# Kernel optimization log

Hardware: AMD Instinct MI355X
Metric: run time of the kernel (lower is better)

Reference implementation:

```python
import jax, jax.numpy as jnp
import numpy as np


def setup_inputs() -> dict:
    key = jax.random.key(0)
    ks = jax.random.split(key, 5)
    b, f, h, w, c = 2, 16, 64, 64, 256
    heads, D = 8, 32
    hD = heads * D
    x = jax.random.normal(ks[0], (b, f, h, w, c), dtype=jnp.float32)
    s = 1.0 / np.sqrt(c)
    Wq = jax.random.normal(ks[1], (c, hD), dtype=jnp.float32) * s
    Wk = jax.random.normal(ks[2], (c, hD), dtype=jnp.float32) * s
    Wv = jax.random.normal(ks[3], (c, hD), dtype=jnp.float32) * s
    Wo = jax.random.normal(ks[4], (hD, c), dtype=jnp.float32) * s
    return {"x": x, "Wq": Wq, "Wk": Wk, "Wv": Wv, "Wo": Wo, "heads": heads}


def reference(x, Wq, Wk, Wv, Wo, heads):
    b, f, h, w, c = x.shape
    hD = Wq.shape[1]
    D = hD // heads
    n = h * w
    # fuse batch & frames; 1x1 conv == channel matmul
    xf = x.reshape(b * f, n, c)  # [(bf), n, c]

    def proj(W):
        # [(bf), n, hD] -> [(bf), heads, D, n]
        p = jnp.einsum('bnc,cd->bnd', xf, W)
        return p.reshape(b * f, n, heads, D).transpose(0, 2, 3, 1)

    q = jax.nn.softmax(proj(Wq), axis=-2)  # softmax over D (note: scale is dead code in source)
    k = jax.nn.softmax(proj(Wk), axis=-1)  # softmax over spatial n
    v = proj(Wv)
    context = jnp.einsum('bhdn,bhen->bhde', k, v)      # [(bf), heads, D, D]
    out = jnp.einsum('bhde,bhdn->bhen', context, q)    # [(bf), heads, D, n]
    out = out.transpose(0, 3, 1, 2).reshape(b * f, n, hD)
    out = jnp.einsum('bnd,dc->bnc', out, Wo)
    return out.reshape(b, f, h, w, c)
```

## Files before the change

kernel.cpp:

```cpp
#include <hip/hip_runtime.h>
#include <hip/hip_bf16.h>


typedef __attribute__((ext_vector_type(8))) short bf16x8;
typedef __attribute__((ext_vector_type(4))) float f32x4;

__device__ __forceinline__ unsigned short f2bf(float x) {
  __hip_bfloat16 h = __float2bfloat16(x);
  union { __hip_bfloat16 b; unsigned short u; } c; c.b = h; return c.u;
}

__global__ __launch_bounds__(256) void k0_prep(const float* __restrict__ Wq,
                                               const float* __restrict__ Wk,
                                               const float* __restrict__ Wv,
                                               unsigned short* __restrict__ WqT,
                                               unsigned short* __restrict__ WkvT) {
  int r = blockIdx.x, c = threadIdx.x;
  if (r < 256)      WqT [(r      )*256 + c] = f2bf(Wq[c*256 + r]);
  else if (r < 512) WkvT[(r - 256)*256 + c] = f2bf(Wk[c*256 + (r-256)]);
  else              WkvT[(r - 256)*256 + c] = f2bf(Wv[c*256 + (r-512)]);
}

__global__ __launch_bounds__(1024, 4) void k1w(const float* __restrict__ x,
                                               const unsigned short* __restrict__ WkvT,
                                               float* __restrict__ ctxp) {
  __shared__ unsigned short As[2][32*256];
  __shared__ unsigned short slab[512*40];
  int bid = blockIdx.x;
  size_t rowbase = (size_t)bid * 256;
  int tid = threadIdx.x;
  int lane = tid & 63, w = tid >> 6;
  int cl = lane & 15, rq = (lane >> 4) << 2, fs = lane >> 4;
  int h = w & 7;
  bool isV = w >= 8;

  bf16x8 bfr[2][8];
#pragma unroll
  for (int ni = 0; ni < 2; ++ni)
#pragma unroll
    for (int kk = 0; kk < 8; ++kk)
      bfr[ni][kk] = *(const bf16x8*)(WkvT + (size_t)(w*32 + ni*16 + cl)*256 + kk*32 + fs*8);

  f32x4 c2[2] = {};
  float dena0 = 0.f, dena1 = 0.f;

  int ar = tid >> 5, as_ = tid & 31;
  int aw = ar*256 + ((as_ ^ (ar & 7)) << 3);
  const float* ap = x + (rowbase + ar)*256 + as_*8;

  int ca0 = h*32 + cl, ca1 = h*32 + 16 + cl;
  int cb  = 256 + h*32 + (isV ? 16 : 0) + cl;
  int ra0 = ca0*40 + fs*8;
  int ra1 = ca1*40 + fs*8;
  int rb  = cb*40  + fs*8;

  f32x4 acc[2][2];

  auto stageA = [&](int buf, float4 v0, float4 v1) {
    unsigned short* Ab = &As[buf][0];
    union { ushort4 u4[2]; int4 i4; } pk;
    pk.u4[0].x = f2bf(v0.x); pk.u4[0].y = f2bf(v0.y); pk.u4[0].z = f2bf(v0.z); pk.u4[0].w = f2bf(v0.w);
    pk.u4[1].x = f2bf(v1.x); pk.u4[1].y = f2bf(v1.y); pk.u4[1].z = f2bf(v1.z); pk.u4[1].w = f2bf(v1.w);
    *(int4*)(&Ab[aw]) = pk.i4;
  };
  auto mainMFMA = [&](int buf) {
    unsigned short* Ab = &As[buf][0];
#pragma unroll
    for (int m = 0; m < 2; ++m)
#pragma unroll
      for (int ni = 0; ni < 2; ++ni) acc[m][ni] = (f32x4){};
#pragma unroll
    for (int kk = 0; kk < 8; ++kk) {
      int so = (((kk*4 + fs) ^ (cl & 7)) << 3);
      bf16x8 a0 = *(const bf16x8*)(&Ab[cl*256 + so]);
      bf16x8 a1 = *(const bf16x8*)(&Ab[(16 + cl)*256 + so]);
#pragma unroll
      for (int ni = 0; ni < 2; ++ni) {
        acc[0][ni] = __builtin_amdgcn_mfma_f32_16x16x32_bf16(a0, bfr[ni][kk], acc[0][ni], 0, 0, 0);
        acc[1][ni] = __builtin_amdgcn_mfma_f32_16x16x32_bf16(a1, bfr[ni][kk], acc[1][ni], 0, 0, 0);
      }
    }
  };
  auto slabWrite = [&]() {
#pragma unroll
    for (int ni = 0; ni < 2; ++ni) {
      int c = w*32 + ni*16 + cl;
#pragma unroll
      for (int m = 0; m < 2; ++m) {
        int n4 = m*16 + rq;
        ushort4 wv;
        if (!isV) {
          float e0 = __expf(acc[m][ni][0]), e1 = __expf(acc[m][ni][1]);
          float e2 = __expf(acc[m][ni][2]), e3 = __expf(acc[m][ni][3]);
          if (ni == 0) dena0 += (e0 + e1) + (e2 + e3); else dena1 += (e0 + e1) + (e2 + e3);
          wv.x = f2bf(e0); wv.y = f2bf(e1); wv.z = f2bf(e2); wv.w = f2bf(e3);
        } else {
          wv.x = f2bf(acc[m][ni][0]); wv.y = f2bf(acc[m][ni][1]);
          wv.z = f2bf(acc[m][ni][2]); wv.w = f2bf(acc[m][ni][3]);
        }
        *(ushort4*)(&slab[c*40 + n4]) = wv;
      }
    }
  };
  auto ctxMFMA = [&]() {
    bf16x8 af0 = *(const bf16x8*)(&slab[ra0]);
    bf16x8 af1 = *(const bf16x8*)(&slab[ra1]);
    bf16x8 bv  = *(const bf16x8*)(&slab[rb]);
    c2[0] = __builtin_amdgcn_mfma_f32_16x16x32_bf16(af0, bv, c2[0], 0, 0, 0);
    c2[1] = __builtin_amdgcn_mfma_f32_16x16x32_bf16(af1, bv, c2[1], 0, 0, 0);
  };

  float4 pa0 = *(const float4*)ap;
  float4 pa1 = *(const float4*)(ap + 4);
  stageA(0, pa0, pa1);
  {
    const float* apn = ap + 32*256;
    pa0 = *(const float4*)apn;
    pa1 = *(const float4*)(apn + 4);
  }
  __syncthreads();
  mainMFMA(0);

  for (int t = 0; t < 8; ++t) {
    if (t < 7) stageA((t + 1) & 1, pa0, pa1);
    slabWrite();
    __syncthreads();
    if (t < 6) {
      const float* apn = ap + (size_t)(t + 2)*32*256;
      pa0 = *(const float4*)apn;
      pa1 = *(const float4*)(apn + 4);
    }
    ctxMFMA();
    if (t < 7) mainMFMA((t + 1) & 1);
    __syncthreads();
  }

  float* cp = ctxp + ((size_t)bid*8 + h)*1056;
  int ec = isV ? 16 + cl : cl;
#pragma unroll
  for (int di = 0; di < 2; ++di)
#pragma unroll
    for (int r = 0; r < 4; ++r)
      cp[(di*16 + rq + r)*33 + ec] = c2[di][r];
  if (!isV) {
    dena0 += __shfl_xor(dena0, 16); dena0 += __shfl_xor(dena0, 32);
    dena1 += __shfl_xor(dena1, 16); dena1 += __shfl_xor(dena1, 32);
    if (fs == 0) {
      cp[cl*33 + 32]        = dena0;
      cp[(16 + cl)*33 + 32] = dena1;
    }
  }
}

__global__ __launch_bounds__(256) void k2b_w2(const float* __restrict__ ctxp,
                                              const float* __restrict__ Wo,
                                              unsigned short* __restrict__ W2t) {
  __shared__ float clds[32*33];
  int bid = blockIdx.x;
  int h = bid & 7, bfi = bid >> 3;
  int tid = threadIdx.x;
  for (int i = tid; i < 1056; i += 256) {
    float s = 0.f;
#pragma unroll
    for (int p = 0; p < 16; ++p)
      s += ctxp[((size_t)(bfi*16 + p)*8 + h)*1056 + i];
    clds[i] = s;
  }
  __syncthreads();
  float acc[32] = {};
#pragma unroll 4
  for (int e = 0; e < 32; ++e) {
    float w = Wo[(size_t)(h*32 + e)*256 + tid];
#pragma unroll
    for (int d = 0; d < 32; ++d) acc[d] += clds[d*33 + e] * w;
  }
  unsigned short* o = W2t + ((size_t)bfi*256 + tid)*256 + h*32;
#pragma unroll
  for (int d = 0; d < 32; ++d) o[d] = f2bf(acc[d] / clds[d*33 + 32]);
}

__global__ __launch_bounds__(512, 2) void k3s(const float* __restrict__ x,
                                              const unsigned short* __restrict__ WqT,
                                              const unsigned short* __restrict__ W2t,
                                              float* __restrict__ out) {
  __shared__ unsigned short As[2][32*256];
  __shared__ unsigned short Qs[2][32*256];
  int bid = blockIdx.x;
  size_t rowbase = (size_t)bid * 256;
  int bfi = bid >> 4;
  int tid = threadIdx.x;
  int lane = tid & 63, wid = tid >> 6;
  int cl = lane & 15, rq = (lane >> 4) << 2, fs = lane >> 4;

  bf16x8 bq[2][8], bw[2][8];
#pragma unroll
  for (int nf = 0; nf < 2; ++nf)
#pragma unroll
    for (int kk = 0; kk < 8; ++kk) {
      bq[nf][kk] = *(const bf16x8*)(WqT + (size_t)(wid*32 + nf*16 + cl)*256 + kk*32 + fs*8);
      bw[nf][kk] = *(const bf16x8*)(W2t + ((size_t)bfi*256 + wid*32 + nf*16 + cl)*256 + kk*32 + fs*8);
    }

  int ar = tid >> 5, as_ = tid & 31;
  int aw0 = ar*256 + ((as_ ^ (ar & 7)) << 3);
  int aw1 = (16 + ar)*256 + ((as_ ^ (ar & 7)) << 3);
  const float* ap = x + (rowbase + ar)*256 + as_*8;

  int qslotbase = wid*4 + (rq >> 3);
  ushort4 qpk[2][2];

  auto stageA = [&](int buf, float4 v0, float4 v1, float4 v2, float4 v3) {
    unsigned short* Ab = &As[buf][0];
    union { ushort4 u4[2]; int4 i4; } pk;
    pk.u4[0].x = f2bf(v0.x); pk.u4[0].y = f2bf(v0.y); pk.u4[0].z = f2bf(v0.z); pk.u4[0].w = f2bf(v0.w);
    pk.u4[1].x = f2bf(v1.x); pk.u4[1].y = f2bf(v1.y); pk.u4[1].z = f2bf(v1.z); pk.u4[1].w = f2bf(v1.w);
    *(int4*)(&Ab[aw0]) = pk.i4;
    pk.u4[0].x = f2bf(v2.x); pk.u4[0].y = f2bf(v2.y); pk.u4[0].z = f2bf(v2.z); pk.u4[0].w = f2bf(v2.w);
    pk.u4[1].x = f2bf(v3.x); pk.u4[1].y = f2bf(v3.y); pk.u4[1].z = f2bf(v3.z); pk.u4[1].w = f2bf(v3.w);
    *(int4*)(&Ab[aw1]) = pk.i4;
  };
  auto p1soft = [&](int buf) {
    unsigned short* Ab = &As[buf][0];
    f32x4 ql[2][2] = {};
#pragma unroll
    for (int kk = 0; kk < 8; ++kk) {
      int so = (((kk*4 + fs) ^ (cl & 7)) << 3);
      bf16x8 a0 = *(const bf16x8*)(&Ab[cl*256 + so]);
      bf16x8 a1 = *(const bf16x8*)(&Ab[(16 + cl)*256 + so]);
#pragma unroll
      for (int nf = 0; nf < 2; ++nf) {
        ql[0][nf] = __builtin_amdgcn_mfma_f32_16x16x32_bf16(bq[nf][kk], a0, ql[0][nf], 0, 0, 0);
        ql[1][nf] = __builtin_amdgcn_mfma_f32_16x16x32_bf16(bq[nf][kk], a1, ql[1][nf], 0, 0, 0);
      }
    }
#pragma unroll
    for (int m = 0; m < 2; ++m) {
      float e0[4], e1[4]; float s8 = 0.f;
#pragma unroll
      for (int r = 0; r < 4; ++r) { e0[r] = __expf(ql[m][0][r]); e1[r] = __expf(ql[m][1][r]); s8 += e0[r] + e1[r]; }
      float s = s8; s += __shfl_xor(s, 16); s += __shfl_xor(s, 32);
      float inv = 1.0f / s;
      qpk[m][0].x = f2bf(e0[0]*inv); qpk[m][0].y = f2bf(e0[1]*inv); qpk[m][0].z = f2bf(e0[2]*inv); qpk[m][0].w = f2bf(e0[3]*inv);
      qpk[m][1].x = f2bf(e1[0]*inv); qpk[m][1].y = f2bf(e1[1]*inv); qpk[m][1].z = f2bf(e1[2]*inv); qpk[m][1].w = f2bf(e1[3]*inv);
    }
  };
  auto qwrite = [&](int buf) {
    unsigned short* Qb = &Qs[buf][0];
#pragma unroll
    for (int m = 0; m < 2; ++m) {
      int row = m*16 + cl;
#pragma unroll
      for (int nf = 0; nf < 2; ++nf) {
        int slot = qslotbase + nf*2;
        *(ushort4*)(&Qb[row*256 + ((slot ^ (row & 7)) << 3) + (rq & 4)]) = qpk[m][nf];
      }
    }
  };

  float4 pa0 = *(const float4*)ap;
  float4 pa1 = *(const float4*)(ap + 4);
  float4 pa2 = *(const float4*)(ap + 16*256);
  float4 pa3 = *(const float4*)(ap + 16*256 + 4);
  stageA(0, pa0, pa1, pa2, pa3);
  {
    const float* apn = ap + 32*256;
    pa0 = *(const float4*)apn;
    pa1 = *(const float4*)(apn + 4);
    pa2 = *(const float4*)(apn + 16*256);
    pa3 = *(const float4*)(apn + 16*256 + 4);
  }
  __syncthreads();
  p1soft(0);

  for (int t = 0; t < 7; ++t) {
    stageA((t + 1) & 1, pa0, pa1, pa2, pa3);
    qwrite(t & 1);
    __syncthreads();
    if (t < 6) {
      const float* apn = ap + (size_t)(t + 2)*32*256;
      pa0 = *(const float4*)apn;
      pa1 = *(const float4*)(apn + 4);
      pa2 = *(const float4*)(apn + 16*256);
      pa3 = *(const float4*)(apn + 16*256 + 4);
    }
    f32x4 oa[2][2] = {};
    {
      unsigned short* Qb = &Qs[t & 1][0];
#pragma unroll
      for (int kk = 0; kk < 8; ++kk) {
        int so = (((kk*4 + fs) ^ (cl & 7)) << 3);
        bf16x8 q0 = *(const bf16x8*)(&Qb[cl*256 + so]);
        bf16x8 q1 = *(const bf16x8*)(&Qb[(16 + cl)*256 + so]);
#pragma unroll
        for (int nf = 0; nf < 2; ++nf) {
          oa[0][nf] = __builtin_amdgcn_mfma_f32_16x16x32_bf16(bw[nf][kk], q0, oa[0][nf], 0, 0, 0);
          oa[1][nf] = __builtin_amdgcn_mfma_f32_16x16x32_bf16(bw[nf][kk], q1, oa[1][nf], 0, 0, 0);
        }
      }
    }
    p1soft((t + 1) & 1);
#pragma unroll
    for (int m = 0; m < 2; ++m)
#pragma unroll
      for (int nf = 0; nf < 2; ++nf)
        *(f32x4*)(&out[(rowbase + (size_t)t*32 + m*16 + cl)*256 + wid*32 + nf*16 + rq]) = oa[m][nf];
  }
  qwrite(1);
  __syncthreads();
  {
    unsigned short* Qb = &Qs[1][0];
    f32x4 oa[2][2] = {};
#pragma unroll
    for (int kk = 0; kk < 8; ++kk) {
      int so = (((kk*4 + fs) ^ (cl & 7)) << 3);
      bf16x8 q0 = *(const bf16x8*)(&Qb[cl*256 + so]);
      bf16x8 q1 = *(const bf16x8*)(&Qb[(16 + cl)*256 + so]);
#pragma unroll
      for (int nf = 0; nf < 2; ++nf) {
        oa[0][nf] = __builtin_amdgcn_mfma_f32_16x16x32_bf16(bw[nf][kk], q0, oa[0][nf], 0, 0, 0);
        oa[1][nf] = __builtin_amdgcn_mfma_f32_16x16x32_bf16(bw[nf][kk], q1, oa[1][nf], 0, 0, 0);
      }
    }
#pragma unroll
    for (int m = 0; m < 2; ++m)
#pragma unroll
      for (int nf = 0; nf < 2; ++nf)
        *(f32x4*)(&out[(rowbase + (size_t)7*32 + m*16 + cl)*256 + wid*32 + nf*16 + rq]) = oa[m][nf];
  }
}

extern "C" void kernel_launch(void* const* d_in, const int* in_sizes, int n_in,
                              void* d_out, int out_size, void* d_ws, size_t ws_size,
                              hipStream_t stream) {
  const float* x  = (const float*)d_in[0];
  const float* Wq = (const float*)d_in[1];
  const float* Wk = (const float*)d_in[2];
  const float* Wv = (const float*)d_in[3];
  const float* Wo = (const float*)d_in[4];
  float* out = (float*)d_out;

  unsigned short* WkvT = (unsigned short*)d_ws;
  unsigned short* WqT  = WkvT + 131072;
  unsigned short* W2t  = WqT  + 65536;
  float*          ctxp = (float*)(W2t + 2097152);

  k0_prep <<<768,  256,  0, stream>>>(Wq, Wk, Wv, WqT, WkvT);
  k1w     <<<512,  1024, 0, stream>>>(x, WkvT, ctxp);
  k2b_w2  <<<256,  256,  0, stream>>>(ctxp, Wo, W2t);
  k3s     <<<512,  512,  0, stream>>>(x, WqT, W2t, out);
}
```

Measured before the change: 143.8 us.

## Double-buffer k1w slab, halve k1w grid to 512 rows per block

Each k1w block now processes 512 spatial rows over 16 chunks instead of 256 over 8, and the grid is halved. The K/V slab is double-buffered, which removes the second barrier per iteration so the context MFMA and the next chunk's projection can overlap. An empty asm ties the preloaded weight fragments to VGPRs so they stay live across the loop. The reduction kernel now sums 8 partial contexts per frame instead of 16. The tradeoffs are more shared memory per block and only 256 blocks to fill the GPU.

```diff
diff --git a/kernel.cpp b/kernel.cpp
--- a/kernel.cpp
+++ b/kernel.cpp
@@ -25,9 +25,9 @@
                                                const unsigned short* __restrict__ WkvT,
                                                float* __restrict__ ctxp) {
   __shared__ unsigned short As[2][32*256];
-  __shared__ unsigned short slab[512*40];
+  __shared__ unsigned short slab[2][512*40];
   int bid = blockIdx.x;
-  size_t rowbase = (size_t)bid * 256;
+  size_t rowbase = (size_t)bid * 512;
   int tid = threadIdx.x;
   int lane = tid & 63, w = tid >> 6;
   int cl = lane & 15, rq = (lane >> 4) << 2, fs = lane >> 4;
@@ -40,6 +40,11 @@
 #pragma unroll
     for (int kk = 0; kk < 8; ++kk)
       bfr[ni][kk] = *(const bf16x8*)(WkvT + (size_t)(w*32 + ni*16 + cl)*256 + kk*32 + fs*8);
+#pragma unroll
+  for (int ni = 0; ni < 2; ++ni)
+#pragma unroll
+    for (int kk = 0; kk < 8; ++kk)
+      asm volatile("" : "+v"(bfr[ni][kk]));
 
   f32x4 c2[2] = {};
   float dena0 = 0.f, dena1 = 0.f;
@@ -81,7 +86,8 @@
       }
     }
   };
-  auto slabWrite = [&]() {
+  auto slabWrite = [&](int buf) {
+    unsigned short* sb = &slab[buf][0];
 #pragma unroll
     for (int ni = 0; ni < 2; ++ni) {
       int c = w*32 + ni*16 + cl;
@@ -98,14 +104,15 @@
           wv.x = f2bf(acc[m][ni][0]); wv.y = f2bf(acc[m][ni][1]);
           wv.z = f2bf(acc[m][ni][2]); wv.w = f2bf(acc[m][ni][3]);
         }
-        *(ushort4*)(&slab[c*40 + n4]) = wv;
-      }
-    }
-  };
-  auto ctxMFMA = [&]() {
-    bf16x8 af0 = *(const bf16x8*)(&slab[ra0]);
-    bf16x8 af1 = *(const bf16x8*)(&slab[ra1]);
-    bf16x8 bv  = *(const bf16x8*)(&slab[rb]);
+        *(ushort4*)(&sb[c*40 + n4]) = wv;
+      }
+    }
+  };
+  auto ctxMFMA = [&](int buf) {
+    unsigned short* sb = &slab[buf][0];
+    bf16x8 af0 = *(const bf16x8*)(&sb[ra0]);
+    bf16x8 af1 = *(const bf16x8*)(&sb[ra1]);
+    bf16x8 bv  = *(const bf16x8*)(&sb[rb]);
     c2[0] = __builtin_amdgcn_mfma_f32_16x16x32_bf16(af0, bv, c2[0], 0, 0, 0);
     c2[1] = __builtin_amdgcn_mfma_f32_16x16x32_bf16(af1, bv, c2[1], 0, 0, 0);
   };
@@ -121,19 +128,21 @@
   __syncthreads();
   mainMFMA(0);
 
-  for (int t = 0; t < 8; ++t) {
-    if (t < 7) stageA((t + 1) & 1, pa0, pa1);
-    slabWrite();
+  for (int t = 0; t < 15; ++t) {
+    slabWrite(t & 1);
+    stageA((t + 1) & 1, pa0, pa1);
     __syncthreads();
-    if (t < 6) {
+    if (t < 14) {
       const float* apn = ap + (size_t)(t + 2)*32*256;
       pa0 = *(const float4*)apn;
       pa1 = *(const float4*)(apn + 4);
     }
-    ctxMFMA();
-    if (t < 7) mainMFMA((t + 1) & 1);
-    __syncthreads();
-  }
+    ctxMFMA(t & 1);
+    mainMFMA((t + 1) & 1);
+  }
+  slabWrite(1);
+  __syncthreads();
+  ctxMFMA(1);
 
   float* cp = ctxp + ((size_t)bid*8 + h)*1056;
   int ec = isV ? 16 + cl : cl;
@@ -162,8 +171,8 @@
   for (int i = tid; i < 1056; i += 256) {
     float s = 0.f;
 #pragma unroll
-    for (int p = 0; p < 16; ++p)
-      s += ctxp[((size_t)(bfi*16 + p)*8 + h)*1056 + i];
+    for (int p = 0; p < 8; ++p)
+      s += ctxp[((size_t)(bfi*8 + p)*8 + h)*1056 + i];
     clds[i] = s;
   }
   __syncthreads();
@@ -345,7 +354,7 @@
   float*          ctxp = (float*)(W2t + 2097152);
 
   k0_prep <<<768,  256,  0, stream>>>(Wq, Wk, Wv, WqT, WkvT);
-  k1w     <<<512,  1024, 0, stream>>>(x, WkvT, ctxp);
+  k1w     <<<256,  1024, 0, stream>>>(x, WkvT, ctxp);
   k2b_w2  <<<256,  256,  0, stream>>>(ctxp, Wo, W2t);
   k3s     <<<512,  512,  0, stream>>>(x, WqT, W2t, out);
 }
```

Result: faster. 131.3 us (-8.7%).
